# Kernel tuning notes

Measured on AMD Instinct MI355X. Metric: run time of the kernel, lower is better.

Reference implementation:

```python
import jax, jax.numpy as jnp
import numpy as np

B, S, D = 1, 2048, 2048
H, HK, HD = 32, 8, 64
GROUPS = H // HK
SCALE = float(HD) ** 0.5
NEG = jnp.float32(-1e9)


def setup_inputs() -> dict:
    key = jax.random.key(0)
    ks = jax.random.split(key, 6)
    hidden_states = jax.random.normal(ks[0], (B, S, D), dtype=jnp.float32)
    # RoPE tables: [S, HD//2], half-split convention
    inv_freq = 1.0 / (10000.0 ** (jnp.arange(0, HD, 2, dtype=jnp.float32) / HD))
    angles = jnp.arange(S, dtype=jnp.float32)[:, None] * inv_freq[None, :]
    freqs_cos = jnp.cos(angles)
    freqs_sin = jnp.sin(angles)
    # additive causal mask [S, S]
    causal = jnp.tril(jnp.ones((S, S), dtype=bool))
    atten_mask = jnp.where(causal, jnp.float32(0.0), NEG)
    std = 0.02
    Wq = jax.random.normal(ks[1], (H * HD, D), dtype=jnp.float32) * std
    Wk = jax.random.normal(ks[2], (HK * HD, D), dtype=jnp.float32) * std
    Wv = jax.random.normal(ks[3], (HK * HD, D), dtype=jnp.float32) * std
    Wo = jax.random.normal(ks[4], (D, H * HD), dtype=jnp.float32) * std
    return {"hidden_states": hidden_states, "freqs_cos": freqs_cos,
            "freqs_sin": freqs_sin, "atten_mask": atten_mask,
            "Wq": Wq, "Wk": Wk, "Wv": Wv, "Wo": Wo}


def _rope(x, cos, sin):
    # x: [B, S, h, HD]; cos/sin: [S, HD//2]
    half = x.shape[-1] // 2
    xr, xi = x[..., :half], x[..., half:]
    c = cos[None, :, None, :]
    s = sin[None, :, None, :]
    return jnp.concatenate([xr * c - xi * s, xr * s + xi * c], axis=-1)


def reference(hidden_states, freqs_cos, freqs_sin, atten_mask, Wq, Wk, Wv, Wo):
    b, s, _ = hidden_states.shape
    q = (hidden_states @ Wq.T).reshape(b, s, H, HD)
    k = (hidden_states @ Wk.T).reshape(b, s, HK, HD)
    v = (hidden_states @ Wv.T).reshape(b, s, HK, HD)
    q = _rope(q, freqs_cos, freqs_sin)
    k = _rope(k, freqs_cos, freqs_sin)
    # GQA: repeat kv heads to match query heads
    k_rep = jnp.repeat(k, GROUPS, axis=2)  # [b, s, H, HD]
    v_rep = jnp.repeat(v, GROUPS, axis=2)
    scores = jnp.einsum('bqhd,bkhd->bhqk', q, k_rep) / SCALE
    scores = scores + atten_mask[None, None, :, :]
    attn = jax.nn.softmax(scores, axis=-1)
    y = jnp.einsum('bhqk,bkhd->bqhd', attn, v_rep).reshape(b, s, H * HD)
    y = y @ Wo.T
    return y
```

## Files before the change

kernel.cpp:

```cpp
#include <hip/hip_runtime.h>


typedef __bf16 bf16_t;
typedef __bf16 bf16x8 __attribute__((ext_vector_type(8)));
typedef __bf16 bf16x4 __attribute__((ext_vector_type(4)));
typedef float f32x4 __attribute__((ext_vector_type(4)));
typedef float f32x16 __attribute__((ext_vector_type(16)));

static constexpr int SEQ   = 2048;
static constexpr int DM    = 2048;
static constexpr int NQKV  = 3072;

__device__ __forceinline__ f32x4 mfma16(bf16x8 a, bf16x8 b, f32x4 c) {
  return __builtin_amdgcn_mfma_f32_16x16x32_bf16(a, b, c, 0, 0, 0);
}
__device__ __forceinline__ f32x16 mfma32(bf16x8 a, bf16x8 b, f32x16 c) {
  return __builtin_amdgcn_mfma_f32_32x32x16_bf16(a, b, c, 0, 0, 0);
}
__device__ __forceinline__ unsigned packbf2(float a, float b) {
  union { bf16_t h[2]; unsigned u; } cv;
  cv.h[0] = (bf16_t)a; cv.h[1] = (bf16_t)b;
  return cv.u;
}
__device__ __forceinline__ void perm32swap(unsigned &a, unsigned &b) {
  asm("v_permlane32_swap_b32 %0, %1" : "+v"(a), "+v"(b));
}
__device__ __forceinline__ bf16x8 ldg8(const bf16_t* p) {
  return *reinterpret_cast<const bf16x8*>(p);
}
__device__ __forceinline__ void gll16(const bf16_t* g, bf16_t* l) {
  __builtin_amdgcn_global_load_lds(
      (const __attribute__((address_space(1))) void*)g,
      (__attribute__((address_space(3))) void*)l, 16, 0, 0);
}

__global__ __launch_bounds__(256) void cast5_kernel(
    const float* __restrict__ s0, const float* __restrict__ s1,
    const float* __restrict__ s2, const float* __restrict__ s3,
    const float* __restrict__ s4,
    bf16_t* __restrict__ d0, bf16_t* __restrict__ d1, bf16_t* __restrict__ d2,
    bf16_t* __restrict__ d3, bf16_t* __restrict__ d4) {
  int i = blockIdx.x * 256 + threadIdx.x;
  const int stride = gridDim.x * 256;
  for (; i < 3670016; i += stride) {
    const float* src; bf16_t* dst; int off; float f = 1.0f;
    if (i < 1048576)      { src = s0; dst = d0; off = i; }
    else if (i < 2097152) { src = s1; dst = d1; off = i - 1048576; f = 0.18033688011112042f; }
    else if (i < 2359296) { src = s2; dst = d2; off = i - 2097152; }
    else if (i < 2621440) { src = s3; dst = d3; off = i - 2359296; }
    else                  { src = s4; dst = d4; off = i - 2621440; }
    float4 v = reinterpret_cast<const float4*>(src)[i < 1048576 ? i :
                 (i < 2097152 ? i - 1048576 : (i < 2359296 ? i - 2097152 :
                 (i < 2621440 ? i - 2359296 : i - 2621440)))];
    (void)off;
    bf16x4 o;
    o[0] = (bf16_t)(v.x * f); o[1] = (bf16_t)(v.y * f);
    o[2] = (bf16_t)(v.z * f); o[3] = (bf16_t)(v.w * f);
    reinterpret_cast<bf16x4*>(dst)[i < 1048576 ? i :
                 (i < 2097152 ? i - 1048576 : (i < 2359296 ? i - 2097152 :
                 (i < 2621440 ? i - 2359296 : i - 2621440)))] = o;
  }
}

template <bool F32OUT>
__global__ __launch_bounds__(256, 3) void gemm_bt(const bf16_t* __restrict__ A,
                                                  const bf16_t* __restrict__ B,
                                                  bf16_t* __restrict__ Cb,
                                                  float* __restrict__ Cf,
                                                  int M, int N, int K) {
  __shared__ __align__(16) bf16_t As[2][64 * 64];
  __shared__ __align__(16) bf16_t Bs[2][128 * 64];
  const int t  = threadIdx.x;
  const int w  = t >> 6;
  const int lr = t & 15;
  const int hi = (t & 63) >> 4;
  const int wr = w >> 1;
  const int wc = w & 1;
  const int rowBase = blockIdx.y * 64;
  const int colBase = blockIdx.x * 128;

  f32x4 acc[2][4] = {};

  const bf16_t* pA[2];
  const bf16_t* pB[4];
#pragma unroll
  for (int i = 0; i < 2; ++i) {
    int s = i * 256 + t, r = s >> 3, cc = ((s & 7) ^ (r & 7)) << 3;
    pA[i] = A + (size_t)(rowBase + r) * K + cc;
  }
#pragma unroll
  for (int i = 0; i < 4; ++i) {
    int s = i * 256 + t, r = s >> 3, cc = ((s & 7) ^ (r & 7)) << 3;
    pB[i] = B + (size_t)(colBase + r) * K + cc;
  }

  auto stage = [&](int buf, int k0) {
#pragma unroll
    for (int i = 0; i < 2; ++i)
      gll16(pA[i] + k0, &As[buf][(i * 256 + w * 64) * 8]);
#pragma unroll
    for (int i = 0; i < 4; ++i)
      gll16(pB[i] + k0, &Bs[buf][(i * 256 + w * 64) * 8]);
  };

  stage(0, 0);
  __syncthreads();
  const int nk = K >> 6;
  for (int ti = 0; ti < nk; ++ti) {
    if (ti + 1 < nk) stage((ti + 1) & 1, (ti + 1) << 6);
    const bf16_t* Ab = &As[ti & 1][0];
    const bf16_t* Bb = &Bs[ti & 1][0];
#pragma unroll
    for (int kh = 0; kh < 2; ++kh) {
      bf16x8 af[2], bfr[4];
#pragma unroll
      for (int m = 0; m < 2; ++m) {
        int R = wr * 32 + m * 16 + lr;
        af[m] = ldg8(&Ab[R * 64 + (((kh * 4 + hi) ^ (R & 7)) << 3)]);
      }
#pragma unroll
      for (int n = 0; n < 4; ++n) {
        int R = wc * 64 + n * 16 + lr;
        bfr[n] = ldg8(&Bb[R * 64 + (((kh * 4 + hi) ^ (R & 7)) << 3)]);
      }
      __builtin_amdgcn_s_setprio(1);
#pragma unroll
      for (int m = 0; m < 2; ++m)
#pragma unroll
        for (int n = 0; n < 4; ++n)
          acc[m][n] = mfma16(af[m], bfr[n], acc[m][n]);
      __builtin_amdgcn_s_setprio(0);
    }
    __syncthreads();
  }

#pragma unroll
  for (int m = 0; m < 2; ++m) {
#pragma unroll
    for (int n = 0; n < 4; ++n) {
      int row0 = rowBase + wr * 32 + m * 16 + hi * 4;
      int col  = colBase + wc * 64 + n * 16 + lr;
#pragma unroll
      for (int r = 0; r < 4; ++r) {
        size_t idx = (size_t)(row0 + r) * N + col;
        if (F32OUT) Cf[idx] = acc[m][n][r];
        else        Cb[idx] = (bf16_t)acc[m][n][r];
      }
    }
  }
}

__global__ __launch_bounds__(256) void ropevt_kernel(bf16_t* __restrict__ qkv,
                                                     const float* __restrict__ fcos,
                                                     const float* __restrict__ fsin,
                                                     bf16_t* __restrict__ vt) {
  int b = blockIdx.x;
  int t = threadIdx.x;
  if (b < SEQ) {
    int s = b;
    const float* cr = fcos + (size_t)s * 32;
    const float* sr = fsin + (size_t)s * 32;
    for (int i = t; i < 1024; i += 256) {
      int h = i >> 5, j = i & 31;
      size_t base = (size_t)s * NQKV + h * 64 + j;
      float xr = (float)qkv[base], xi = (float)qkv[base + 32];
      float c = cr[j], sn = sr[j];
      qkv[base]      = (bf16_t)(xr * c - xi * sn);
      qkv[base + 32] = (bf16_t)(xr * sn + xi * c);
    }
    {
      int h = t >> 5, j = t & 31;
      size_t base = (size_t)s * NQKV + 2048 + h * 64 + j;
      float xr = (float)qkv[base], xi = (float)qkv[base + 32];
      float c = cr[j], sn = sr[j];
      qkv[base]      = (bf16_t)(xr * c - xi * sn);
      qkv[base + 32] = (bf16_t)(xr * sn + xi * c);
    }
  } else {
    int i = b - SEQ;
    for (int s = t; s < SEQ; s += 256)
      vt[(size_t)i * SEQ + s] = qkv[(size_t)s * NQKV + 2560 + i];
  }
}

__global__ __launch_bounds__(256, 2) void attn_kernel(const bf16_t* __restrict__ qkv,
                                                      const bf16_t* __restrict__ vt,
                                                      bf16_t* __restrict__ attn) {
  __shared__ __align__(16) bf16_t smem[2][2][64 * 64];
  const int t  = threadIdx.x;
  const int w  = t >> 6;
  const int l  = t & 63;
  const int qc = l & 31;
  const int h5 = l >> 5;
  const int u  = blockIdx.x * 4 + w;
  const int h  = u & 31;
  const int jj = u >> 5;
  const int qt = (jj & 1) ? (63 - (jj >> 1)) : (jj >> 1);
  const int hk = h >> 2;
  const int q0 = qt * 32;

  const bf16_t* qrow = qkv + (size_t)(q0 + qc) * NQKV + h * 64 + h5 * 8;
  bf16x8 qf[4];
#pragma unroll
  for (int ks = 0; ks < 4; ++ks) qf[ks] = ldg8(qrow + ks * 16);

  f32x16 o[2] = {};
  float l_r = 0.f;
  const float M0 = 16.0f;

  const bf16_t* gk[2];
  const bf16_t* gv[2];
#pragma unroll
  for (int i = 0; i < 2; ++i) {
    int s = i * 256 + t, r = s >> 3, cc = ((s & 7) ^ (r & 7)) << 3;
    gk[i] = qkv + 2048 + hk * 64 + (size_t)r * NQKV + cc;
    gv[i] = vt + (size_t)(hk * 64 + r) * SEQ + cc;
  }

  auto stageT = [&](int buf, int kv0) {
#pragma unroll
    for (int i = 0; i < 2; ++i) {
      gll16(gk[i] + (size_t)kv0 * NQKV, &smem[buf][0][(i * 256 + w * 64) * 8]);
      gll16(gv[i] + kv0, &smem[buf][1][(i * 256 + w * 64) * 8]);
    }
  };

  auto packhalf = [&](const float (&pp)[16], bf16x8 &b0, bf16x8 &b1) {
    unsigned pw[8];
#pragma unroll
    for (int i2 = 0; i2 < 8; ++i2) pw[i2] = packbf2(pp[2 * i2], pp[2 * i2 + 1]);
    perm32swap(pw[0], pw[2]); perm32swap(pw[1], pw[3]);
    perm32swap(pw[4], pw[6]); perm32swap(pw[5], pw[7]);
    union { unsigned u4[4]; bf16x8 v; } c0 = {{pw[0], pw[1], pw[2], pw[3]}};
    union { unsigned u4[4]; bf16x8 v; } c1v = {{pw[4], pw[5], pw[6], pw[7]}};
    b0 = c0.v; b1 = c1v.v;
  };

  const int xq = qc & 7;
  const int nt = (q0 >> 6) + 1;

  stageT(0, 0);
  __syncthreads();

  for (int ti = 0; ti < nt; ++ti) {
    const int kv0 = ti << 6;
    if (ti + 1 < nt) stageT((ti + 1) & 1, (ti + 1) << 6);
    const bf16_t* Kt  = &smem[ti & 1][0][0];
    const bf16_t* Vtl = &smem[ti & 1][1][0];

    const bool h1act = (kv0 + 32 <= q0);
    const bool diag0 = (kv0 == q0);
    const bool diag1 = (kv0 + 32 == q0);

    f32x16 s0v = {}, s1v = {};
    __builtin_amdgcn_s_setprio(1);
#pragma unroll
    for (int ks = 0; ks < 4; ++ks) {
      bf16x8 kf = ldg8(&Kt[qc * 64 + (((2 * ks + h5) ^ xq) << 3)]);
      s0v = mfma32(kf, qf[ks], s0v);
    }
    if (h1act) {
#pragma unroll
      for (int ks = 0; ks < 4; ++ks) {
        bf16x8 kf = ldg8(&Kt[(32 + qc) * 64 + (((2 * ks + h5) ^ xq) << 3)]);
        s1v = mfma32(kf, qf[ks], s1v);
      }
    }
    __builtin_amdgcn_s_setprio(0);

    float p0[16], p1[16];
    float sm = 0.f;
#pragma unroll
    for (int r = 0; r < 16; ++r) {
      float sv = s0v[r];
      if (diag0) {
        int krow = (r & 3) + 8 * (r >> 2) + 4 * h5;
        if (krow > qc) sv = -1e30f;
      }
      p0[r] = exp2f(sv - M0);
      sm += p0[r];
    }
    if (h1act) {
#pragma unroll
      for (int r = 0; r < 16; ++r) {
        float sv = s1v[r];
        if (diag1) {
          int krow = (r & 3) + 8 * (r >> 2) + 4 * h5;
          if (krow > qc) sv = -1e30f;
        }
        p1[r] = exp2f(sv - M0);
        sm += p1[r];
      }
    }
    l_r += sm;

    bf16x8 pb0, pb1;
    packhalf(p0, pb0, pb1);
    __builtin_amdgcn_s_setprio(1);
    o[0] = mfma32(ldg8(&Vtl[qc * 64 + ((h5 ^ xq) << 3)]), pb0, o[0]);
    o[0] = mfma32(ldg8(&Vtl[qc * 64 + (((2 + h5) ^ xq) << 3)]), pb1, o[0]);
    o[1] = mfma32(ldg8(&Vtl[(32 + qc) * 64 + ((h5 ^ xq) << 3)]), pb0, o[1]);
    o[1] = mfma32(ldg8(&Vtl[(32 + qc) * 64 + (((2 + h5) ^ xq) << 3)]), pb1, o[1]);
    __builtin_amdgcn_s_setprio(0);
    if (h1act) {
      bf16x8 pb2, pb3;
      packhalf(p1, pb2, pb3);
      __builtin_amdgcn_s_setprio(1);
      o[0] = mfma32(ldg8(&Vtl[qc * 64 + (((4 + h5) ^ xq) << 3)]), pb2, o[0]);
      o[0] = mfma32(ldg8(&Vtl[qc * 64 + (((6 + h5) ^ xq) << 3)]), pb3, o[0]);
      o[1] = mfma32(ldg8(&Vtl[(32 + qc) * 64 + (((4 + h5) ^ xq) << 3)]), pb2, o[1]);
      o[1] = mfma32(ldg8(&Vtl[(32 + qc) * 64 + (((6 + h5) ^ xq) << 3)]), pb3, o[1]);
      __builtin_amdgcn_s_setprio(0);
    }
    __syncthreads();
  }

  float ltot = l_r + __shfl_xor(l_r, 32);
  float inv = 1.0f / ltot;
  bf16_t* L = &smem[0][0][0] + w * (32 * 72);
#pragma unroll
  for (int dt = 0; dt < 2; ++dt)
#pragma unroll
    for (int rq = 0; rq < 4; ++rq) {
      bf16x4 v4;
#pragma unroll
      for (int e = 0; e < 4; ++e) v4[e] = (bf16_t)(o[dt][rq * 4 + e] * inv);
      *reinterpret_cast<bf16x4*>(&L[qc * 72 + dt * 32 + rq * 8 + h5 * 4]) = v4;
    }
#pragma unroll
  for (int p = 0; p < 8; ++p) {
    int idx = p * 256 + l * 4;
    int q   = idx >> 6;
    int d0  = idx & 63;
    bf16x4 v4 = *reinterpret_cast<const bf16x4*>(&L[q * 72 + d0]);
    *reinterpret_cast<bf16x4*>(&attn[(size_t)(q0 + q) * DM + h * 64 + d0]) = v4;
  }
}

extern "C" void kernel_launch(void* const* d_in, const int* in_sizes, int n_in,
                              void* d_out, int out_size, void* d_ws, size_t ws_size,
                              hipStream_t stream) {
  const float* hidden = (const float*)d_in[0];
  const float* fcos   = (const float*)d_in[1];
  const float* fsin   = (const float*)d_in[2];
  const float* Wq = (const float*)d_in[4];
  const float* Wk = (const float*)d_in[5];
  const float* Wv = (const float*)d_in[6];
  const float* Wo = (const float*)d_in[7];
  float* out = (float*)d_out;

  char* ws = (char*)d_ws;
  bf16_t* Xbf  = (bf16_t*)(ws);
  bf16_t* Wall = (bf16_t*)(ws + ((size_t)8 << 20));
  bf16_t* Wobf = (bf16_t*)(ws + ((size_t)20 << 20));
  bf16_t* QKV  = (bf16_t*)(ws + ((size_t)28 << 20));
  bf16_t* Vt   = (bf16_t*)(ws + ((size_t)40 << 20));
  bf16_t* Attn = (bf16_t*)(ws + ((size_t)42 << 20));
  if (ws_size < ((size_t)50 << 20)) return;

  cast5_kernel<<<2048, 256, 0, stream>>>(hidden, Wq, Wk, Wv, Wo,
                                         Xbf, Wall, Wall + (size_t)2048 * 2048,
                                         Wall + (size_t)2560 * 2048, Wobf);

  dim3 g1(NQKV / 128, SEQ / 64);
  gemm_bt<false><<<g1, 256, 0, stream>>>(Xbf, Wall, QKV, nullptr, SEQ, NQKV, DM);

  ropevt_kernel<<<SEQ + 512, 256, 0, stream>>>(QKV, fcos, fsin, Vt);

  attn_kernel<<<512, 256, 0, stream>>>(QKV, Vt, Attn);

  dim3 g2(DM / 128, SEQ / 64);
  gemm_bt<true><<<g2, 256, 0, stream>>>(Attn, Wobf, nullptr, out, SEQ, DM, DM);
}
```

Measured before the change: 244.5 us.

## Fuse RoPE and V-transpose into 32x32 MFMA GEMM; split attention KV across wave halves

The QKV projection GEMM now uses 128x128 tiles with 32x32x16 MFMA. Its epilogue applies RoPE and writes V transposed, so the separate rope/transpose kernel and its extra pass over QKV are gone. The attention kernel now processes 32-key tiles, and the causal KV range is split between two wave pairs that are merged through LDS at the end. This doubles the grid and raises occupancy to 4 blocks. In exchange it adds an LDS reduction and a different tile schedule. The output GEMM also moves to the larger-tile MFMA32 form.

```diff
diff --git a/kernel.cpp b/kernel.cpp
--- a/kernel.cpp
+++ b/kernel.cpp
@@ -11,9 +11,6 @@
 static constexpr int DM    = 2048;
 static constexpr int NQKV  = 3072;
 
-__device__ __forceinline__ f32x4 mfma16(bf16x8 a, bf16x8 b, f32x4 c) {
-  return __builtin_amdgcn_mfma_f32_16x16x32_bf16(a, b, c, 0, 0, 0);
-}
 __device__ __forceinline__ f32x16 mfma32(bf16x8 a, bf16x8 b, f32x16 c) {
   return __builtin_amdgcn_mfma_f32_32x32x16_bf16(a, b, c, 0, 0, 0);
 }
@@ -43,161 +40,159 @@
   int i = blockIdx.x * 256 + threadIdx.x;
   const int stride = gridDim.x * 256;
   for (; i < 3670016; i += stride) {
-    const float* src; bf16_t* dst; int off; float f = 1.0f;
-    if (i < 1048576)      { src = s0; dst = d0; off = i; }
+    const float* src; bf16_t* dst; int off = i; float f = 1.0f;
+    if (i < 1048576)      { src = s0; dst = d0; }
     else if (i < 2097152) { src = s1; dst = d1; off = i - 1048576; f = 0.18033688011112042f; }
     else if (i < 2359296) { src = s2; dst = d2; off = i - 2097152; }
     else if (i < 2621440) { src = s3; dst = d3; off = i - 2359296; }
     else                  { src = s4; dst = d4; off = i - 2621440; }
-    float4 v = reinterpret_cast<const float4*>(src)[i < 1048576 ? i :
-                 (i < 2097152 ? i - 1048576 : (i < 2359296 ? i - 2097152 :
-                 (i < 2621440 ? i - 2359296 : i - 2621440)))];
-    (void)off;
+    float4 v = reinterpret_cast<const float4*>(src)[off];
     bf16x4 o;
     o[0] = (bf16_t)(v.x * f); o[1] = (bf16_t)(v.y * f);
     o[2] = (bf16_t)(v.z * f); o[3] = (bf16_t)(v.w * f);
-    reinterpret_cast<bf16x4*>(dst)[i < 1048576 ? i :
-                 (i < 2097152 ? i - 1048576 : (i < 2359296 ? i - 2097152 :
-                 (i < 2621440 ? i - 2359296 : i - 2621440)))] = o;
-  }
-}
-
-template <bool F32OUT>
-__global__ __launch_bounds__(256, 3) void gemm_bt(const bf16_t* __restrict__ A,
-                                                  const bf16_t* __restrict__ B,
-                                                  bf16_t* __restrict__ Cb,
-                                                  float* __restrict__ Cf,
-                                                  int M, int N, int K) {
-  __shared__ __align__(16) bf16_t As[2][64 * 64];
+    reinterpret_cast<bf16x4*>(dst)[off] = o;
+  }
+}
+
+template <int MODE>
+__global__ __launch_bounds__(256, 2) void gemm32(const bf16_t* __restrict__ A,
+                                                 const bf16_t* __restrict__ B,
+                                                 float* __restrict__ Cf,
+                                                 bf16_t* __restrict__ QKV,
+                                                 bf16_t* __restrict__ Vt,
+                                                 const float* __restrict__ fcos,
+                                                 const float* __restrict__ fsin,
+                                                 int N, int K) {
+  __shared__ __align__(16) bf16_t As[2][128 * 64];
   __shared__ __align__(16) bf16_t Bs[2][128 * 64];
-  const int t  = threadIdx.x;
-  const int w  = t >> 6;
-  const int lr = t & 15;
-  const int hi = (t & 63) >> 4;
-  const int wr = w >> 1;
-  const int wc = w & 1;
-  const int rowBase = blockIdx.y * 64;
-  const int colBase = blockIdx.x * 128;
-
-  f32x4 acc[2][4] = {};
-
-  const bf16_t* pA[2];
-  const bf16_t* pB[4];
-#pragma unroll
-  for (int i = 0; i < 2; ++i) {
-    int s = i * 256 + t, r = s >> 3, cc = ((s & 7) ^ (r & 7)) << 3;
-    pA[i] = A + (size_t)(rowBase + r) * K + cc;
-  }
-#pragma unroll
-  for (int i = 0; i < 4; ++i) {
-    int s = i * 256 + t, r = s >> 3, cc = ((s & 7) ^ (r & 7)) << 3;
-    pB[i] = B + (size_t)(colBase + r) * K + cc;
-  }
-
-  auto stage = [&](int buf, int k0) {
-#pragma unroll
-    for (int i = 0; i < 2; ++i)
-      gll16(pA[i] + k0, &As[buf][(i * 256 + w * 64) * 8]);
-#pragma unroll
-    for (int i = 0; i < 4; ++i)
-      gll16(pB[i] + k0, &Bs[buf][(i * 256 + w * 64) * 8]);
-  };
-
-  stage(0, 0);
-  __syncthreads();
-  const int nk = K >> 6;
-  for (int ti = 0; ti < nk; ++ti) {
-    if (ti + 1 < nk) stage((ti + 1) & 1, (ti + 1) << 6);
-    const bf16_t* Ab = &As[ti & 1][0];
-    const bf16_t* Bb = &Bs[ti & 1][0];
-#pragma unroll
-    for (int kh = 0; kh < 2; ++kh) {
-      bf16x8 af[2], bfr[4];
-#pragma unroll
-      for (int m = 0; m < 2; ++m) {
-        int R = wr * 32 + m * 16 + lr;
-        af[m] = ldg8(&Ab[R * 64 + (((kh * 4 + hi) ^ (R & 7)) << 3)]);
-      }
-#pragma unroll
-      for (int n = 0; n < 4; ++n) {
-        int R = wc * 64 + n * 16 + lr;
-        bfr[n] = ldg8(&Bb[R * 64 + (((kh * 4 + hi) ^ (R & 7)) << 3)]);
-      }
-      __builtin_amdgcn_s_setprio(1);
-#pragma unroll
-      for (int m = 0; m < 2; ++m)
-#pragma unroll
-        for (int n = 0; n < 4; ++n)
-          acc[m][n] = mfma16(af[m], bfr[n], acc[m][n]);
-      __builtin_amdgcn_s_setprio(0);
-    }
-    __syncthreads();
-  }
-
-#pragma unroll
-  for (int m = 0; m < 2; ++m) {
-#pragma unroll
-    for (int n = 0; n < 4; ++n) {
-      int row0 = rowBase + wr * 32 + m * 16 + hi * 4;
-      int col  = colBase + wc * 64 + n * 16 + lr;
-#pragma unroll
-      for (int r = 0; r < 4; ++r) {
-        size_t idx = (size_t)(row0 + r) * N + col;
-        if (F32OUT) Cf[idx] = acc[m][n][r];
-        else        Cb[idx] = (bf16_t)acc[m][n][r];
-      }
-    }
-  }
-}
-
-__global__ __launch_bounds__(256) void ropevt_kernel(bf16_t* __restrict__ qkv,
-                                                     const float* __restrict__ fcos,
-                                                     const float* __restrict__ fsin,
-                                                     bf16_t* __restrict__ vt) {
-  int b = blockIdx.x;
-  int t = threadIdx.x;
-  if (b < SEQ) {
-    int s = b;
-    const float* cr = fcos + (size_t)s * 32;
-    const float* sr = fsin + (size_t)s * 32;
-    for (int i = t; i < 1024; i += 256) {
-      int h = i >> 5, j = i & 31;
-      size_t base = (size_t)s * NQKV + h * 64 + j;
-      float xr = (float)qkv[base], xi = (float)qkv[base + 32];
-      float c = cr[j], sn = sr[j];
-      qkv[base]      = (bf16_t)(xr * c - xi * sn);
-      qkv[base + 32] = (bf16_t)(xr * sn + xi * c);
-    }
-    {
-      int h = t >> 5, j = t & 31;
-      size_t base = (size_t)s * NQKV + 2048 + h * 64 + j;
-      float xr = (float)qkv[base], xi = (float)qkv[base + 32];
-      float c = cr[j], sn = sr[j];
-      qkv[base]      = (bf16_t)(xr * c - xi * sn);
-      qkv[base + 32] = (bf16_t)(xr * sn + xi * c);
-    }
-  } else {
-    int i = b - SEQ;
-    for (int s = t; s < SEQ; s += 256)
-      vt[(size_t)i * SEQ + s] = qkv[(size_t)s * NQKV + 2560 + i];
-  }
-}
-
-__global__ __launch_bounds__(256, 2) void attn_kernel(const bf16_t* __restrict__ qkv,
-                                                      const bf16_t* __restrict__ vt,
-                                                      bf16_t* __restrict__ attn) {
-  __shared__ __align__(16) bf16_t smem[2][2][64 * 64];
   const int t  = threadIdx.x;
   const int w  = t >> 6;
   const int l  = t & 63;
   const int qc = l & 31;
   const int h5 = l >> 5;
-  const int u  = blockIdx.x * 4 + w;
-  const int h  = u & 31;
-  const int jj = u >> 5;
-  const int qt = (jj & 1) ? (63 - (jj >> 1)) : (jj >> 1);
-  const int hk = h >> 2;
+  const int wr = w >> 1;
+  const int wc = w & 1;
+  const int rowBase = blockIdx.y * 128;
+  const int colBase = blockIdx.x * 128;
+
+  f32x16 acc[2][2] = {};
+
+  const bf16_t* pA[4];
+  const bf16_t* pB[4];
+#pragma unroll
+  for (int i = 0; i < 4; ++i) {
+    int s = i * 256 + t, r = s >> 3, cc = ((s & 7) ^ (r & 7)) << 3;
+    pA[i] = A + (size_t)(rowBase + r) * K + cc;
+    pB[i] = B + (size_t)(colBase + r) * K + cc;
+  }
+  auto stage = [&](int buf, int k0) {
+#pragma unroll
+    for (int i = 0; i < 4; ++i)
+      gll16(pA[i] + k0, &As[buf][(i * 256 + w * 64) * 8]);
+#pragma unroll
+    for (int i = 0; i < 4; ++i)
+      gll16(pB[i] + k0, &Bs[buf][(i * 256 + w * 64) * 8]);
+  };
+
+  stage(0, 0);
+  __syncthreads();
+  const int nk = K >> 6;
+  const int xq = qc & 7;
+  for (int ti = 0; ti < nk; ++ti) {
+    if (ti + 1 < nk) stage((ti + 1) & 1, (ti + 1) << 6);
+    const bf16_t* Ab = &As[ti & 1][0];
+    const bf16_t* Bb = &Bs[ti & 1][0];
+#pragma unroll
+    for (int ks = 0; ks < 4; ++ks) {
+      const int ch = ((ks * 2 + h5) ^ xq) << 3;
+      bf16x8 af[2], bfr[2];
+#pragma unroll
+      for (int m = 0; m < 2; ++m)
+        af[m] = ldg8(&Ab[(wr * 64 + m * 32 + qc) * 64 + ch]);
+#pragma unroll
+      for (int n = 0; n < 2; ++n)
+        bfr[n] = ldg8(&Bb[(wc * 64 + n * 32 + qc) * 64 + ch]);
+      __builtin_amdgcn_s_setprio(1);
+#pragma unroll
+      for (int m = 0; m < 2; ++m)
+#pragma unroll
+        for (int n = 0; n < 2; ++n)
+          acc[m][n] = mfma32(af[m], bfr[n], acc[m][n]);
+      __builtin_amdgcn_s_setprio(0);
+    }
+    __syncthreads();
+  }
+
+  if (MODE == 0) {
+#pragma unroll
+    for (int m = 0; m < 2; ++m)
+#pragma unroll
+      for (int n = 0; n < 2; ++n) {
+        int col = colBase + wc * 64 + n * 32 + qc;
+#pragma unroll
+        for (int rr = 0; rr < 4; ++rr)
+#pragma unroll
+          for (int j = 0; j < 4; ++j) {
+            int row = rowBase + wr * 64 + m * 32 + rr * 8 + h5 * 4 + j;
+            Cf[(size_t)row * N + col] = acc[m][n][rr * 4 + j];
+          }
+      }
+  } else {
+    const int cb = colBase + wc * 64;
+    if (colBase < 2560) {
+#pragma unroll
+      for (int m = 0; m < 2; ++m)
+#pragma unroll
+        for (int rr = 0; rr < 4; ++rr)
+#pragma unroll
+          for (int j = 0; j < 4; ++j) {
+            int row = rowBase + wr * 64 + m * 32 + rr * 8 + h5 * 4 + j;
+            float c = fcos[row * 32 + qc];
+            float s = fsin[row * 32 + qc];
+            float xr = acc[m][0][rr * 4 + j];
+            float xi = acc[m][1][rr * 4 + j];
+            QKV[(size_t)row * NQKV + cb + qc]      = (bf16_t)(xr * c - xi * s);
+            QKV[(size_t)row * NQKV + cb + 32 + qc] = (bf16_t)(xr * s + xi * c);
+          }
+    } else {
+#pragma unroll
+      for (int m = 0; m < 2; ++m)
+#pragma unroll
+        for (int n = 0; n < 2; ++n) {
+          int col = cb + n * 32 + qc - 2560;
+#pragma unroll
+          for (int rr = 0; rr < 4; ++rr) {
+            int row0 = rowBase + wr * 64 + m * 32 + rr * 8 + h5 * 4;
+            bf16x4 v4;
+#pragma unroll
+            for (int j = 0; j < 4; ++j) v4[j] = (bf16_t)acc[m][n][rr * 4 + j];
+            *reinterpret_cast<bf16x4*>(&Vt[(size_t)col * SEQ + row0]) = v4;
+          }
+        }
+    }
+  }
+}
+
+__global__ __launch_bounds__(256, 4) void attn_kernel(const bf16_t* __restrict__ qkv,
+                                                      const bf16_t* __restrict__ vt,
+                                                      bf16_t* __restrict__ attn) {
+  __shared__ __align__(16) bf16_t smem[2][2][2][32 * 64];
+  const int t  = threadIdx.x;
+  const int w  = t >> 6;
+  const int l  = t & 63;
+  const int qc = l & 31;
+  const int h5 = l >> 5;
+  const int b  = blockIdx.x;
+  const int qt = 63 - (b >> 4);
+  const int hk = b & 7;
+  const int pr = (b >> 3) & 1;
+  const int half = w >> 1;
+  const int h  = hk * 4 + pr * 2 + (w & 1);
   const int q0 = qt * 32;
+  const int nT = qt + 1;
+  const int n0 = (nT + 1) >> 1;
+  const int myN = half ? (nT - n0) : n0;
+  const int myBase = half ? n0 : 0;
 
   const bf16_t* qrow = qkv + (size_t)(q0 + qc) * NQKV + h * 64 + h5 * 8;
   bf16x8 qf[4];
@@ -208,132 +203,112 @@
   float l_r = 0.f;
   const float M0 = 16.0f;
 
-  const bf16_t* gk[2];
-  const bf16_t* gv[2];
-#pragma unroll
-  for (int i = 0; i < 2; ++i) {
-    int s = i * 256 + t, r = s >> 3, cc = ((s & 7) ^ (r & 7)) << 3;
-    gk[i] = qkv + 2048 + hk * 64 + (size_t)r * NQKV + cc;
-    gv[i] = vt + (size_t)(hk * 64 + r) * SEQ + cc;
-  }
-
-  auto stageT = [&](int buf, int kv0) {
-#pragma unroll
-    for (int i = 0; i < 2; ++i) {
-      gll16(gk[i] + (size_t)kv0 * NQKV, &smem[buf][0][(i * 256 + w * 64) * 8]);
-      gll16(gv[i] + kv0, &smem[buf][1][(i * 256 + w * 64) * 8]);
+  const int rK = t >> 3, cK = ((t & 7) ^ (rK & 7)) << 3;
+  const int rV = t >> 2, cV = ((t & 3) ^ (rV & 3)) << 3;
+  const bf16_t* gK = qkv + 2048 + hk * 64 + (size_t)rK * NQKV + cK;
+  const bf16_t* gV = vt + (size_t)(hk * 64 + rV) * SEQ + cV;
+
+  auto stageT = [&](int buf, int i0, int i1) {
+    if (i0 < n0) {
+      gll16(gK + (size_t)(i0 * 32) * NQKV, &smem[0][buf][0][t * 8]);
+      gll16(gV + i0 * 32,                  &smem[0][buf][1][t * 8]);
+    }
+    if (i1 < nT) {
+      gll16(gK + (size_t)(i1 * 32) * NQKV, &smem[1][buf][0][t * 8]);
+      gll16(gV + i1 * 32,                  &smem[1][buf][1][t * 8]);
     }
   };
 
-  auto packhalf = [&](const float (&pp)[16], bf16x8 &b0, bf16x8 &b1) {
-    unsigned pw[8];
-#pragma unroll
-    for (int i2 = 0; i2 < 8; ++i2) pw[i2] = packbf2(pp[2 * i2], pp[2 * i2 + 1]);
-    perm32swap(pw[0], pw[2]); perm32swap(pw[1], pw[3]);
-    perm32swap(pw[4], pw[6]); perm32swap(pw[5], pw[7]);
-    union { unsigned u4[4]; bf16x8 v; } c0 = {{pw[0], pw[1], pw[2], pw[3]}};
-    union { unsigned u4[4]; bf16x8 v; } c1v = {{pw[4], pw[5], pw[6], pw[7]}};
-    b0 = c0.v; b1 = c1v.v;
-  };
-
   const int xq = qc & 7;
-  const int nt = (q0 >> 6) + 1;
-
-  stageT(0, 0);
+  const int xv = qc & 3;
+
+  stageT(0, 0, n0);
   __syncthreads();
 
-  for (int ti = 0; ti < nt; ++ti) {
-    const int kv0 = ti << 6;
-    if (ti + 1 < nt) stageT((ti + 1) & 1, (ti + 1) << 6);
-    const bf16_t* Kt  = &smem[ti & 1][0][0];
-    const bf16_t* Vtl = &smem[ti & 1][1][0];
-
-    const bool h1act = (kv0 + 32 <= q0);
-    const bool diag0 = (kv0 == q0);
-    const bool diag1 = (kv0 + 32 == q0);
-
-    f32x16 s0v = {}, s1v = {};
-    __builtin_amdgcn_s_setprio(1);
-#pragma unroll
-    for (int ks = 0; ks < 4; ++ks) {
-      bf16x8 kf = ldg8(&Kt[qc * 64 + (((2 * ks + h5) ^ xq) << 3)]);
-      s0v = mfma32(kf, qf[ks], s0v);
-    }
-    if (h1act) {
-#pragma unroll
-      for (int ks = 0; ks < 4; ++ks) {
-        bf16x8 kf = ldg8(&Kt[(32 + qc) * 64 + (((2 * ks + h5) ^ xq) << 3)]);
-        s1v = mfma32(kf, qf[ks], s1v);
+  for (int rr = 0; rr < n0; ++rr) {
+    stageT((rr + 1) & 1, rr + 1, n0 + rr + 1);
+    if (rr < myN) {
+      const int myIdx = myBase + rr;
+      const bf16_t* Kt = &smem[half][rr & 1][0][0];
+      const bf16_t* Vl = &smem[half][rr & 1][1][0];
+      const bool diag = (myIdx == qt);
+
+      f32x16 sv = {};
+      __builtin_amdgcn_s_setprio(1);
+#pragma unroll
+      for (int ks = 0; ks < 4; ++ks)
+        sv = mfma32(ldg8(&Kt[qc * 64 + (((ks * 2 + h5) ^ xq) << 3)]), qf[ks], sv);
+      __builtin_amdgcn_s_setprio(0);
+
+      float p[16];
+      float sm = 0.f;
+#pragma unroll
+      for (int r = 0; r < 16; ++r) {
+        float x = sv[r];
+        if (diag) {
+          int krow = (r & 3) + 8 * (r >> 2) + 4 * h5;
+          if (krow > qc) x = -1e30f;
+        }
+        p[r] = exp2f(x - M0);
+        sm += p[r];
       }
-    }
-    __builtin_amdgcn_s_setprio(0);
-
-    float p0[16], p1[16];
-    float sm = 0.f;
-#pragma unroll
-    for (int r = 0; r < 16; ++r) {
-      float sv = s0v[r];
-      if (diag0) {
-        int krow = (r & 3) + 8 * (r >> 2) + 4 * h5;
-        if (krow > qc) sv = -1e30f;
+      l_r += sm;
+
+      unsigned pw[8];
+#pragma unroll
+      for (int i2 = 0; i2 < 8; ++i2) pw[i2] = packbf2(p[2 * i2], p[2 * i2 + 1]);
+      perm32swap(pw[0], pw[2]); perm32swap(pw[1], pw[3]);
+      perm32swap(pw[4], pw[6]); perm32swap(pw[5], pw[7]);
+      union { unsigned u4[4]; bf16x8 v; } c0 = {{pw[0], pw[1], pw[2], pw[3]}};
+      union { unsigned u4[4]; bf16x8 v; } c1 = {{pw[4], pw[5], pw[6], pw[7]}};
+
+      __builtin_amdgcn_s_setprio(1);
+      o[0] = mfma32(ldg8(&Vl[qc * 32 + ((h5 ^ xv) << 3)]), c0.v, o[0]);
+      o[0] = mfma32(ldg8(&Vl[qc * 32 + (((2 + h5) ^ xv) << 3)]), c1.v, o[0]);
+      o[1] = mfma32(ldg8(&Vl[(32 + qc) * 32 + ((h5 ^ xv) << 3)]), c0.v, o[1]);
+      o[1] = mfma32(ldg8(&Vl[(32 + qc) * 32 + (((2 + h5) ^ xv) << 3)]), c1.v, o[1]);
+      __builtin_amdgcn_s_setprio(0);
+    }
+    __syncthreads();
+  }
+
+  float* MG = (float*)&smem[0][0][0][0];
+  float* R  = MG + (w & 1) * 2112;
+  if (half == 1) {
+#pragma unroll
+    for (int dt = 0; dt < 2; ++dt)
+#pragma unroll
+      for (int r = 0; r < 16; ++r) R[(dt * 16 + r) * 64 + l] = o[dt][r];
+    R[2048 + l] = l_r;
+  }
+  __syncthreads();
+  if (half == 0) {
+#pragma unroll
+    for (int dt = 0; dt < 2; ++dt)
+#pragma unroll
+      for (int r = 0; r < 16; ++r) o[dt][r] += R[(dt * 16 + r) * 64 + l];
+    l_r += R[2048 + l];
+    float ltot = l_r + __shfl_xor(l_r, 32);
+    float inv = 1.0f / ltot;
+
+    bf16_t* L = (bf16_t*)R;
+#pragma unroll
+    for (int dt = 0; dt < 2; ++dt)
+#pragma unroll
+      for (int rq = 0; rq < 4; ++rq) {
+        bf16x4 v4;
+#pragma unroll
+        for (int e = 0; e < 4; ++e) v4[e] = (bf16_t)(o[dt][rq * 4 + e] * inv);
+        *reinterpret_cast<bf16x4*>(&L[qc * 72 + dt * 32 + rq * 8 + h5 * 4]) = v4;
       }
-      p0[r] = exp2f(sv - M0);
-      sm += p0[r];
-    }
-    if (h1act) {
-#pragma unroll
-      for (int r = 0; r < 16; ++r) {
-        float sv = s1v[r];
-        if (diag1) {
-          int krow = (r & 3) + 8 * (r >> 2) + 4 * h5;
-          if (krow > qc) sv = -1e30f;
-        }
-        p1[r] = exp2f(sv - M0);
-        sm += p1[r];
-      }
-    }
-    l_r += sm;
-
-    bf16x8 pb0, pb1;
-    packhalf(p0, pb0, pb1);
-    __builtin_amdgcn_s_setprio(1);
-    o[0] = mfma32(ldg8(&Vtl[qc * 64 + ((h5 ^ xq) << 3)]), pb0, o[0]);
-    o[0] = mfma32(ldg8(&Vtl[qc * 64 + (((2 + h5) ^ xq) << 3)]), pb1, o[0]);
-    o[1] = mfma32(ldg8(&Vtl[(32 + qc) * 64 + ((h5 ^ xq) << 3)]), pb0, o[1]);
-    o[1] = mfma32(ldg8(&Vtl[(32 + qc) * 64 + (((2 + h5) ^ xq) << 3)]), pb1, o[1]);
-    __builtin_amdgcn_s_setprio(0);
-    if (h1act) {
-      bf16x8 pb2, pb3;
-      packhalf(p1, pb2, pb3);
-      __builtin_amdgcn_s_setprio(1);
-      o[0] = mfma32(ldg8(&Vtl[qc * 64 + (((4 + h5) ^ xq) << 3)]), pb2, o[0]);
-      o[0] = mfma32(ldg8(&Vtl[qc * 64 + (((6 + h5) ^ xq) << 3)]), pb3, o[0]);
-      o[1] = mfma32(ldg8(&Vtl[(32 + qc) * 64 + (((4 + h5) ^ xq) << 3)]), pb2, o[1]);
-      o[1] = mfma32(ldg8(&Vtl[(32 + qc) * 64 + (((6 + h5) ^ xq) << 3)]), pb3, o[1]);
-      __builtin_amdgcn_s_setprio(0);
-    }
-    __syncthreads();
-  }
-
-  float ltot = l_r + __shfl_xor(l_r, 32);
-  float inv = 1.0f / ltot;
-  bf16_t* L = &smem[0][0][0] + w * (32 * 72);
-#pragma unroll
-  for (int dt = 0; dt < 2; ++dt)
-#pragma unroll
-    for (int rq = 0; rq < 4; ++rq) {
-      bf16x4 v4;
-#pragma unroll
-      for (int e = 0; e < 4; ++e) v4[e] = (bf16_t)(o[dt][rq * 4 + e] * inv);
-      *reinterpret_cast<bf16x4*>(&L[qc * 72 + dt * 32 + rq * 8 + h5 * 4]) = v4;
-    }
-#pragma unroll
-  for (int p = 0; p < 8; ++p) {
-    int idx = p * 256 + l * 4;
-    int q   = idx >> 6;
-    int d0  = idx & 63;
-    bf16x4 v4 = *reinterpret_cast<const bf16x4*>(&L[q * 72 + d0]);
-    *reinterpret_cast<bf16x4*>(&attn[(size_t)(q0 + q) * DM + h * 64 + d0]) = v4;
+#pragma unroll
+    for (int p = 0; p < 8; ++p) {
+      int idx = p * 256 + l * 4;
+      int q   = idx >> 6;
+      int d0  = idx & 63;
+      bf16x4 v4 = *reinterpret_cast<const bf16x4*>(&L[q * 72 + d0]);
+      *reinterpret_cast<bf16x4*>(&attn[(size_t)(q0 + q) * DM + h * 64 + d0]) = v4;
+    }
   }
 }
 
@@ -362,13 +337,13 @@
                                          Xbf, Wall, Wall + (size_t)2048 * 2048,
                                          Wall + (size_t)2560 * 2048, Wobf);
 
-  dim3 g1(NQKV / 128, SEQ / 64);
-  gemm_bt<false><<<g1, 256, 0, stream>>>(Xbf, Wall, QKV, nullptr, SEQ, NQKV, DM);
-
-  ropevt_kernel<<<SEQ + 512, 256, 0, stream>>>(QKV, fcos, fsin, Vt);
-
-  attn_kernel<<<512, 256, 0, stream>>>(QKV, Vt, Attn);
-
-  dim3 g2(DM / 128, SEQ / 64);
-  gemm_bt<true><<<g2, 256, 0, stream>>>(Attn, Wobf, nullptr, out, SEQ, DM, DM);
-}
+  dim3 g1(NQKV / 128, SEQ / 128);
+  gemm32<1><<<g1, 256, 0, stream>>>(Xbf, Wall, nullptr, QKV, Vt, fcos, fsin,
+                                    NQKV, DM);
+
+  attn_kernel<<<1024, 256, 0, stream>>>(QKV, Vt, Attn);
+
+  dim3 g2(DM / 128, SEQ / 128);
+  gemm32<0><<<g2, 256, 0, stream>>>(Attn, Wobf, out, nullptr, nullptr, nullptr,
+                                    nullptr, DM, DM);
+}
```

After: 232.8 us. 4.8% less time.
